# Performance work log

Hardware: AMD Instinct MI355X
Metric: run time of the kernel (lower is better)

Reference implementation:

```python
import jax, jax.numpy as jnp
import numpy as np

EPS = 1e-5
SLOPE = 0.01  # torch LeakyReLU default negative_slope


def _stage(h, W):
    # h: [B, N, k, Cin]; W: [Cout, Cin] (1x1 conv, no bias)
    h = jnp.einsum('bnkc,oc->bnko', h, W)
    # InstanceNorm2d (affine=False): normalize per (batch, channel) over spatial (N, k)
    mean = jnp.mean(h, axis=(1, 2), keepdims=True)
    var = jnp.var(h, axis=(1, 2), keepdims=True)
    h = (h - mean) * jax.lax.rsqrt(var + EPS)
    return jnp.where(h >= 0, h, SLOPE * h)


def setup_inputs() -> dict:
    key = jax.random.key(0)
    k1, k2, k3, k4, k5 = jax.random.split(key, 5)
    B, N, D, K, C = 8, 4096, 64, 20, 64
    x = jax.random.normal(k1, (B, N, D), dtype=jnp.float32)
    ind = jax.random.randint(k2, (B, N, K), 0, B * N, dtype=jnp.int64)
    W1 = jax.random.normal(k3, (C, 2 * D), dtype=jnp.float32) * 0.05
    W2 = jax.random.normal(k4, (C, C), dtype=jnp.float32) * 0.05
    W3 = jax.random.normal(k5, (C, C), dtype=jnp.float32) * 0.05
    return {"x": x, "ind": ind, "W1": W1, "W2": W2, "W3": W3}


def reference(x, ind, W1, W2, W3):
    B, N, D = x.shape
    k = ind.shape[2]
    # Gather neighbors via global (B*N) indices, as in the torch code
    y = x.reshape(B * N, D)[ind.reshape(B * N, k)].reshape(B, N, k, D)  # [B,N,k,D]
    xe = jnp.broadcast_to(x[:, :, None, :], (B, N, k, D))
    feat = jnp.concatenate([y - xe, xe], axis=3)  # [B,N,k,2D]
    h = _stage(feat, W1)
    h = _stage(h, W2)
    h = _stage(h, W3)
    # max-pool over k neighbors -> [B, N, Cout]
    return jnp.max(h, axis=2)
```

## Files before the change

kernel.cpp:

```cpp
#include <hip/hip_runtime.h>

#define BDIM 8
#define NPTS 4096
#define KNEI 20
#define BN (BDIM*NPTS)
#define NKCNT (NPTS*KNEI)
#define EPSI 1e-5f
#define SLOPE 0.01f

typedef _Float16 half_t;
typedef __attribute__((ext_vector_type(2))) _Float16 h2v;
typedef __attribute__((ext_vector_type(4))) _Float16 h4v;
typedef __attribute__((ext_vector_type(8))) _Float16 h8v;
typedef __attribute__((ext_vector_type(4))) float f32x4;
typedef __attribute__((ext_vector_type(2))) float f32x2;

__device__ __forceinline__ h2v cvt2(float a, float b) {
    return __builtin_bit_cast(h2v, __builtin_amdgcn_cvt_pkrtz(a, b));
}
__device__ __forceinline__ unsigned long long pack4_f16(const f32x4& a) {
    unsigned p0 = __builtin_bit_cast(unsigned, cvt2(a[0], a[1]));
    unsigned p1 = __builtin_bit_cast(unsigned, cvt2(a[2], a[3]));
    return ((unsigned long long)p1 << 32) | p0;
}

__global__ __launch_bounds__(256) void k0_uv(const float* __restrict__ x,
        const float* __restrict__ W1, const float* __restrict__ W2,
        const float* __restrict__ W3, half_t* __restrict__ u,
        half_t* __restrict__ v, half_t* __restrict__ Wh2,
        half_t* __restrict__ Wh3) {
    int tid = threadIdx.x;
    if (blockIdx.x >= BN / 16) {
        const float* src = (blockIdx.x == BN / 16) ? W2 : W3;
        half_t* dst = (blockIdx.x == BN / 16) ? Wh2 : Wh3;
        for (int i = tid; i < 4096; i += 256) dst[i] = (half_t)src[i];
        return;
    }
    __shared__ float wlds[64 * 129];
    __shared__ float xs[16 * 64];
    int m0 = blockIdx.x * 16;
    for (int i = tid; i < 8192; i += 256)
        wlds[(i >> 7) * 129 + (i & 127)] = W1[i];
    for (int i = tid; i < 1024; i += 256)
        xs[i] = x[m0 * 64 + i];
    __syncthreads();
    int o = tid & 63;
    int r0 = tid >> 6;
    float au[4] = {0.f, 0.f, 0.f, 0.f};
    float av[4] = {0.f, 0.f, 0.f, 0.f};
    for (int c = 0; c < 64; ++c) {
        float wa = wlds[o * 129 + c];
        float wb = wlds[o * 129 + 64 + c];
        float wd = wb - wa;
#pragma unroll
        for (int jj = 0; jj < 4; ++jj) {
            float xv = xs[(r0 + jj * 4) * 64 + c];
            au[jj] += xv * wa;
            av[jj] += xv * wd;
        }
    }
#pragma unroll
    for (int jj = 0; jj < 4; ++jj) {
        int m = m0 + r0 + jj * 4;
        u[(size_t)m * 64 + o] = (half_t)au[jj];
        v[(size_t)m * 64 + o] = (half_t)av[jj];
    }
}

__global__ __launch_bounds__(256) void k1_stats1(const half_t* __restrict__ u,
        const half_t* __restrict__ v, const int* __restrict__ ind,
        float* __restrict__ s1) {
    __shared__ float sacc[128];
    int tid = threadIdx.x;
    if (tid < 128) sacc[tid] = 0.f;
    int lane = tid & 63, w = tid >> 6;
    int b = blockIdx.x >> 8;
    int n0 = (blockIdx.x & 255) << 4;
    int p = b * NPTS + n0 + w * 4 + (lane >> 4);
    int rh = (lane >> 3) & 1, c8 = lane & 7;
    h8v vv = *(const h8v*)(v + (size_t)p * 64 + c8 * 8);
    const int* ip = ind + (size_t)p * 20;
    float s[8] = {}, qa[8] = {};
#pragma unroll
    for (int r = 0; r < 10; ++r) {
        int idx = ip[r * 2 + rh];
        h8v uu = *(const h8v*)(u + (size_t)idx * 64 + c8 * 8);
        h8v h = uu + vv;
#pragma unroll
        for (int j = 0; j < 8; ++j) {
            float f = (float)h[j];
            s[j] += f; qa[j] = fmaf(f, f, qa[j]);
        }
    }
#pragma unroll
    for (int m = 8; m <= 32; m <<= 1)
#pragma unroll
        for (int j = 0; j < 8; ++j) {
            s[j] += __shfl_xor(s[j], m, 64);
            qa[j] += __shfl_xor(qa[j], m, 64);
        }
    __syncthreads();
    if ((lane & 56) == 0) {
#pragma unroll
        for (int j = 0; j < 8; ++j) {
            atomicAdd(&sacc[c8 * 8 + j], s[j]);
            atomicAdd(&sacc[64 + c8 * 8 + j], qa[j]);
        }
    }
    __syncthreads();
    if (tid < 128)
        atomicAdd(&s1[(tid >> 6) * 512 + b * 64 + (tid & 63)], sacc[tid]);
}

__global__ __launch_bounds__(256, 4) void k2_stats2(const half_t* __restrict__ u,
        const half_t* __restrict__ v, const int* __restrict__ ind,
        const half_t* __restrict__ Wh2, const float* __restrict__ s1,
        float* __restrict__ s2) {
    __shared__ float sacc[128];
    int tid = threadIdx.x;
    if (tid < 128) sacc[tid] = 0.f;
    int lane = tid & 63, w = tid >> 6;
    int l15 = lane & 15, q = lane >> 4;
    int b = blockIdx.x >> 8;
    int n0 = (blockIdx.x & 255) << 4;
    int base = b * NPTS + n0;
    int base20 = base * 20;
    h8v aw[4][2];
#pragma unroll
    for (int mt = 0; mt < 4; ++mt)
#pragma unroll
        for (int kc = 0; kc < 2; ++kc)
            aw[mt][kc] = *(const h8v*)(Wh2 + (mt * 16 + l15) * 64 + kc * 32 + q * 8);
    const float inv = 1.0f / (float)NKCNT;
    h8v r1v[2], m1v[2];
#pragma unroll
    for (int kc = 0; kc < 2; ++kc)
#pragma unroll
        for (int j = 0; j < 8; ++j) {
            int c = kc * 32 + q * 8 + j;
            float mm = s1[b * 64 + c] * inv;
            float va = s1[512 + b * 64 + c] * inv - mm * mm;
            float rs = rsqrtf(va + EPSI);
            r1v[kc][j] = (half_t)rs;
            m1v[kc][j] = (half_t)(-mm * rs);
        }
    int gp = base + w * 4 + (l15 >> 2);
    h8v vfr[2];
#pragma unroll
    for (int kc = 0; kc < 2; ++kc)
        vfr[kc] = *(const h8v*)(v + (size_t)gp * 64 + kc * 32 + q * 8);
    int idxs[5];
#pragma unroll
    for (int nt = 0; nt < 5; ++nt)
        idxs[nt] = ind[base20 + w * 80 + l15 * 5 + nt];
    float ss[4][4] = {}, sq[4][4] = {};
#pragma unroll
    for (int nt = 0; nt < 5; ++nt) {
        const half_t* up = u + (size_t)idxs[nt] * 64;
        h8v bfr[2];
#pragma unroll
        for (int kc = 0; kc < 2; ++kc) {
            h8v uu = *(const h8v*)(up + kc * 32 + q * 8);
            h8v h = uu + vfr[kc];
            h8v t = h * r1v[kc] + m1v[kc];
            bfr[kc] = __builtin_elementwise_max(t, t * (half_t)SLOPE);
        }
#pragma unroll
        for (int mt = 0; mt < 4; ++mt) {
            f32x4 a = {0.f, 0.f, 0.f, 0.f};
            a = __builtin_amdgcn_mfma_f32_16x16x32_f16(aw[mt][0], bfr[0], a, 0, 0, 0);
            a = __builtin_amdgcn_mfma_f32_16x16x32_f16(aw[mt][1], bfr[1], a, 0, 0, 0);
#pragma unroll
            for (int j = 0; j < 4; ++j) {
                ss[mt][j] += a[j];
                sq[mt][j] = fmaf(a[j], a[j], sq[mt][j]);
            }
        }
    }
#pragma unroll
    for (int m = 1; m < 16; m <<= 1)
#pragma unroll
        for (int mt = 0; mt < 4; ++mt)
#pragma unroll
            for (int j = 0; j < 4; ++j) {
                ss[mt][j] += __shfl_xor(ss[mt][j], m, 64);
                sq[mt][j] += __shfl_xor(sq[mt][j], m, 64);
            }
    __syncthreads();
    if (l15 == 0) {
#pragma unroll
        for (int mt = 0; mt < 4; ++mt)
#pragma unroll
            for (int j = 0; j < 4; ++j) {
                atomicAdd(&sacc[mt * 16 + q * 4 + j], ss[mt][j]);
                atomicAdd(&sacc[64 + mt * 16 + q * 4 + j], sq[mt][j]);
            }
    }
    __syncthreads();
    if (tid < 128)
        atomicAdd(&s2[(tid >> 6) * 512 + b * 64 + (tid & 63)], sacc[tid]);
}

__global__ __launch_bounds__(256, 4) void k3_fused(const half_t* __restrict__ u,
        const half_t* __restrict__ v, const int* __restrict__ ind,
        const half_t* __restrict__ Wh2, const half_t* __restrict__ Wh3,
        const float* __restrict__ s1, const float* __restrict__ s2,
        float* __restrict__ s3, float* __restrict__ out) {
    __shared__ __align__(16) unsigned char wlds[16384];
    __shared__ __align__(16) unsigned char scr[16384];
    __shared__ float sacc[128];
    int tid = threadIdx.x;
    if (tid < 128) sacc[tid] = 0.f;
    int lane = tid & 63, w = tid >> 6;
    int l15 = lane & 15, q = lane >> 4;
    int rw7 = l15 & 7;
    int b = blockIdx.x >> 8;
    int n0 = (blockIdx.x & 255) << 4;
    int base = b * NPTS + n0;
    int base20 = base * 20;
    for (int i = tid; i < 512; i += 256) {
        int rw = i >> 3, ch = i & 7;
        *(h8v*)(wlds + rw * 128 + ((ch ^ (rw & 7)) << 4)) =
            *(const h8v*)(Wh2 + rw * 64 + ch * 8);
        *(h8v*)(wlds + 8192 + rw * 128 + ((ch ^ (rw & 7)) << 4)) =
            *(const h8v*)(Wh3 + rw * 64 + ch * 8);
    }
    const float inv = 1.0f / (float)NKCNT;
    h8v r1v[2], m1v[2], r2v[2], m2v[2];
#pragma unroll
    for (int kc = 0; kc < 2; ++kc)
#pragma unroll
        for (int j = 0; j < 8; ++j) {
            int c = kc * 32 + q * 8 + j;
            float mm = s1[b * 64 + c] * inv;
            float va = s1[512 + b * 64 + c] * inv - mm * mm;
            float rs = rsqrtf(va + EPSI);
            r1v[kc][j] = (half_t)rs;
            m1v[kc][j] = (half_t)(-mm * rs);
            float mm2 = s2[b * 64 + c] * inv;
            float va2 = s2[512 + b * 64 + c] * inv - mm2 * mm2;
            float rs2 = rsqrtf(va2 + EPSI);
            r2v[kc][j] = (half_t)rs2;
            m2v[kc][j] = (half_t)(-mm2 * rs2);
        }
    int gp = base + w * 4 + (l15 >> 2);
    h8v vfr[2];
#pragma unroll
    for (int kc = 0; kc < 2; ++kc)
        vfr[kc] = *(const h8v*)(v + (size_t)gp * 64 + kc * 32 + q * 8);
    int idxs[5];
#pragma unroll
    for (int nt = 0; nt < 5; ++nt)
        idxs[nt] = ind[base20 + w * 80 + l15 * 5 + nt];
    __syncthreads();
    h8v bf2[5][2];
#pragma unroll
    for (int nt = 0; nt < 5; ++nt) {
        unsigned char* scrw = scr + w * 4096 + (nt & 1) * 2048;
        const half_t* up = u + (size_t)idxs[nt] * 64;
        h8v bfr[2];
#pragma unroll
        for (int kc = 0; kc < 2; ++kc) {
            h8v uu = *(const h8v*)(up + kc * 32 + q * 8);
            h8v h = uu + vfr[kc];
            h8v t = h * r1v[kc] + m1v[kc];
            bfr[kc] = __builtin_elementwise_max(t, t * (half_t)SLOPE);
        }
#pragma unroll
        for (int mt = 0; mt < 4; ++mt) {
            h8v w0 = *(const h8v*)(wlds + (mt * 16 + l15) * 128 + ((q ^ rw7) << 4));
            h8v w1 = *(const h8v*)(wlds + (mt * 16 + l15) * 128 + (((4 + q) ^ rw7) << 4));
            f32x4 a = {0.f, 0.f, 0.f, 0.f};
            a = __builtin_amdgcn_mfma_f32_16x16x32_f16(w0, bfr[0], a, 0, 0, 0);
            a = __builtin_amdgcn_mfma_f32_16x16x32_f16(w1, bfr[1], a, 0, 0, 0);
            *(unsigned long long*)(scrw + l15 * 128 +
                (((mt * 2 + (q >> 1)) ^ rw7) << 4) + (q & 1) * 8) = pack4_f16(a);
        }
#pragma unroll
        for (int kc = 0; kc < 2; ++kc) {
            h8v hv = *(const h8v*)(scrw + l15 * 128 + (((kc * 4 + q) ^ rw7) << 4));
            h8v t = hv * r2v[kc] + m2v[kc];
            bf2[nt][kc] = __builtin_elementwise_max(t, t * (half_t)SLOPE);
        }
    }
    float ss[4][4] = {}, sq[4][4] = {};
    h2v pm[4][2];
#pragma unroll
    for (int mt = 0; mt < 4; ++mt)
#pragma unroll
        for (int r = 0; r < 2; ++r)
            pm[mt][r] = (h2v){(half_t)-65504.f, (half_t)-65504.f};
#pragma unroll
    for (int nt = 0; nt < 5; ++nt) {
#pragma unroll
        for (int mt = 0; mt < 4; ++mt) {
            h8v w0 = *(const h8v*)(wlds + 8192 + (mt * 16 + l15) * 128 + ((q ^ rw7) << 4));
            h8v w1 = *(const h8v*)(wlds + 8192 + (mt * 16 + l15) * 128 + (((4 + q) ^ rw7) << 4));
            f32x4 a = {0.f, 0.f, 0.f, 0.f};
            a = __builtin_amdgcn_mfma_f32_16x16x32_f16(w0, bf2[nt][0], a, 0, 0, 0);
            a = __builtin_amdgcn_mfma_f32_16x16x32_f16(w1, bf2[nt][1], a, 0, 0, 0);
#pragma unroll
            for (int j = 0; j < 4; ++j) {
                ss[mt][j] += a[j];
                sq[mt][j] = fmaf(a[j], a[j], sq[mt][j]);
            }
            h2v p0 = cvt2(a[0], a[1]);
            h2v p1 = cvt2(a[2], a[3]);
            pm[mt][0] = __builtin_elementwise_max(pm[mt][0], p0);
            pm[mt][1] = __builtin_elementwise_max(pm[mt][1], p1);
        }
    }
#pragma unroll
    for (int m = 1; m <= 2; m <<= 1)
#pragma unroll
        for (int mt = 0; mt < 4; ++mt)
#pragma unroll
            for (int r = 0; r < 2; ++r) {
                int t = __shfl_xor(__builtin_bit_cast(int, pm[mt][r]), m, 64);
                pm[mt][r] = __builtin_elementwise_max(pm[mt][r],
                               __builtin_bit_cast(h2v, t));
            }
    {
        int ms = l15 & 3;
        h2v sa = ms == 0 ? pm[0][0] : ms == 1 ? pm[1][0] : ms == 2 ? pm[2][0] : pm[3][0];
        h2v sb = ms == 0 ? pm[0][1] : ms == 1 ? pm[1][1] : ms == 2 ? pm[2][1] : pm[3][1];
        f32x4 o = {(float)sa[0], (float)sa[1], (float)sb[0], (float)sb[1]};
        *(f32x4*)(out + (size_t)gp * 64 + ms * 16 + q * 4) = o;
    }
#pragma unroll
    for (int m = 1; m < 16; m <<= 1)
#pragma unroll
        for (int mt = 0; mt < 4; ++mt)
#pragma unroll
            for (int j = 0; j < 4; ++j) {
                ss[mt][j] += __shfl_xor(ss[mt][j], m, 64);
                sq[mt][j] += __shfl_xor(sq[mt][j], m, 64);
            }
    if (l15 == 0) {
#pragma unroll
        for (int mt = 0; mt < 4; ++mt)
#pragma unroll
            for (int j = 0; j < 4; ++j) {
                atomicAdd(&sacc[mt * 16 + q * 4 + j], ss[mt][j]);
                atomicAdd(&sacc[64 + mt * 16 + q * 4 + j], sq[mt][j]);
            }
    }
    __syncthreads();
    if (tid < 128)
        atomicAdd(&s3[(tid >> 6) * 512 + b * 64 + (tid & 63)], sacc[tid]);
}

__global__ __launch_bounds__(256) void k4_final(float* __restrict__ out,
        const float* __restrict__ s3) {
    int idx = blockIdx.x * 256 + threadIdx.x;
    int c = idx & 63;
    int b = idx >> 18;
    const float inv = 1.0f / (float)NKCNT;
    float mm = s3[b * 64 + c] * inv;
    float vv = s3[512 + b * 64 + c] * inv - mm * mm;
    float r = rsqrtf(vv + EPSI);
    float val = (out[idx] - mm) * r;
    out[idx] = val >= 0.f ? val : SLOPE * val;
}

extern "C" void kernel_launch(void* const* d_in, const int* in_sizes, int n_in,
                              void* d_out, int out_size, void* d_ws, size_t ws_size,
                              hipStream_t stream) {
    const float* x   = (const float*)d_in[0];
    const int*   ind = (const int*)d_in[1];
    const float* W1  = (const float*)d_in[2];
    const float* W2  = (const float*)d_in[3];
    const float* W3  = (const float*)d_in[4];
    float* out = (float*)d_out;

    half_t* u   = (half_t*)d_ws;
    half_t* v   = u + (size_t)BN * 64;
    half_t* Wh2 = v + (size_t)BN * 64;
    half_t* Wh3 = Wh2 + 4096;
    float* stats = (float*)(Wh3 + 4096);
    float* s1 = stats;
    float* s2 = stats + 1024;
    float* s3 = stats + 2048;

    (void)hipMemsetAsync(stats, 0, 3 * 1024 * sizeof(float), stream);
    k0_uv<<<dim3(BN / 16 + 2), dim3(256), 0, stream>>>(x, W1, W2, W3, u, v, Wh2, Wh3);
    k1_stats1<<<dim3(BN / 16), dim3(256), 0, stream>>>(u, v, ind, s1);
    k2_stats2<<<dim3(BN / 16), dim3(256), 0, stream>>>(u, v, ind, Wh2, s1, s2);
    k3_fused<<<dim3(BN / 16), dim3(256), 0, stream>>>(u, v, ind, Wh2, Wh3, s1, s2, s3, out);
    k4_final<<<dim3(BN * 64 / 256), dim3(256), 0, stream>>>(out, s3);
}
```

Measured before the change: 185.6 us.

## Use MFMA for u/v precompute, batch gathers, keep weights in registers

After: 192.3 us. 1.04x slower.

```diff
diff --git a/kernel.cpp b/kernel.cpp
--- a/kernel.cpp
+++ b/kernel.cpp
@@ -30,40 +30,53 @@
         half_t* __restrict__ v, half_t* __restrict__ Wh2,
         half_t* __restrict__ Wh3) {
     int tid = threadIdx.x;
-    if (blockIdx.x >= BN / 16) {
-        const float* src = (blockIdx.x == BN / 16) ? W2 : W3;
-        half_t* dst = (blockIdx.x == BN / 16) ? Wh2 : Wh3;
+    if (blockIdx.x >= BN / 64) {
+        const float* src = (blockIdx.x == BN / 64) ? W2 : W3;
+        half_t* dst = (blockIdx.x == BN / 64) ? Wh2 : Wh3;
         for (int i = tid; i < 4096; i += 256) dst[i] = (half_t)src[i];
         return;
     }
-    __shared__ float wlds[64 * 129];
-    __shared__ float xs[16 * 64];
-    int m0 = blockIdx.x * 16;
-    for (int i = tid; i < 8192; i += 256)
-        wlds[(i >> 7) * 129 + (i & 127)] = W1[i];
-    for (int i = tid; i < 1024; i += 256)
-        xs[i] = x[m0 * 64 + i];
-    __syncthreads();
-    int o = tid & 63;
-    int r0 = tid >> 6;
-    float au[4] = {0.f, 0.f, 0.f, 0.f};
-    float av[4] = {0.f, 0.f, 0.f, 0.f};
-    for (int c = 0; c < 64; ++c) {
-        float wa = wlds[o * 129 + c];
-        float wb = wlds[o * 129 + 64 + c];
-        float wd = wb - wa;
-#pragma unroll
-        for (int jj = 0; jj < 4; ++jj) {
-            float xv = xs[(r0 + jj * 4) * 64 + c];
-            au[jj] += xv * wa;
-            av[jj] += xv * wd;
-        }
-    }
-#pragma unroll
-    for (int jj = 0; jj < 4; ++jj) {
-        int m = m0 + r0 + jj * 4;
-        u[(size_t)m * 64 + o] = (half_t)au[jj];
-        v[(size_t)m * 64 + o] = (half_t)av[jj];
+    int lane = tid & 63, w = tid >> 6;
+    int l15 = lane & 15, q = lane >> 4;
+    int row = blockIdx.x * 64 + w * 16 + l15;
+    h8v bx[2];
+#pragma unroll
+    for (int kc = 0; kc < 2; ++kc) {
+        const float* xp = x + (size_t)row * 64 + kc * 32 + q * 8;
+        f32x4 x0 = *(const f32x4*)xp;
+        f32x4 x1 = *(const f32x4*)(xp + 4);
+        h8v t;
+#pragma unroll
+        for (int j = 0; j < 4; ++j) { t[j] = (half_t)x0[j]; t[4 + j] = (half_t)x1[j]; }
+        bx[kc] = t;
+    }
+    h8v wa[4][2], wd[4][2];
+#pragma unroll
+    for (int mt = 0; mt < 4; ++mt)
+#pragma unroll
+        for (int kc = 0; kc < 2; ++kc) {
+            const float* wp = W1 + (mt * 16 + l15) * 128 + kc * 32 + q * 8;
+            f32x4 a0 = *(const f32x4*)wp;
+            f32x4 a1 = *(const f32x4*)(wp + 4);
+            f32x4 b0 = *(const f32x4*)(wp + 64);
+            f32x4 b1 = *(const f32x4*)(wp + 68);
+            h8v ta, td;
+#pragma unroll
+            for (int j = 0; j < 4; ++j) {
+                ta[j] = (half_t)a0[j]; ta[4 + j] = (half_t)a1[j];
+                td[j] = (half_t)(b0[j] - a0[j]); td[4 + j] = (half_t)(b1[j] - a1[j]);
+            }
+            wa[mt][kc] = ta; wd[mt][kc] = td;
+        }
+#pragma unroll
+    for (int mt = 0; mt < 4; ++mt) {
+        f32x4 au = {0.f, 0.f, 0.f, 0.f}, av = {0.f, 0.f, 0.f, 0.f};
+        au = __builtin_amdgcn_mfma_f32_16x16x32_f16(wa[mt][0], bx[0], au, 0, 0, 0);
+        au = __builtin_amdgcn_mfma_f32_16x16x32_f16(wa[mt][1], bx[1], au, 0, 0, 0);
+        av = __builtin_amdgcn_mfma_f32_16x16x32_f16(wd[mt][0], bx[0], av, 0, 0, 0);
+        av = __builtin_amdgcn_mfma_f32_16x16x32_f16(wd[mt][1], bx[1], av, 0, 0, 0);
+        *(unsigned long long*)(u + (size_t)row * 64 + mt * 16 + q * 4) = pack4_f16(au);
+        *(unsigned long long*)(v + (size_t)row * 64 + mt * 16 + q * 4) = pack4_f16(av);
     }
 }
 
@@ -78,14 +91,19 @@
     int n0 = (blockIdx.x & 255) << 4;
     int p = b * NPTS + n0 + w * 4 + (lane >> 4);
     int rh = (lane >> 3) & 1, c8 = lane & 7;
+    const int* ip = ind + (size_t)p * 20;
+    int idx[10];
+#pragma unroll
+    for (int r = 0; r < 10; ++r) idx[r] = ip[r * 2 + rh];
     h8v vv = *(const h8v*)(v + (size_t)p * 64 + c8 * 8);
-    const int* ip = ind + (size_t)p * 20;
+    h8v g[10];
+#pragma unroll
+    for (int r = 0; r < 10; ++r)
+        g[r] = *(const h8v*)(u + (size_t)idx[r] * 64 + c8 * 8);
     float s[8] = {}, qa[8] = {};
 #pragma unroll
     for (int r = 0; r < 10; ++r) {
-        int idx = ip[r * 2 + rh];
-        h8v uu = *(const h8v*)(u + (size_t)idx * 64 + c8 * 8);
-        h8v h = uu + vv;
+        h8v h = g[r] + vv;
 #pragma unroll
         for (int j = 0; j < 8; ++j) {
             float f = (float)h[j];
@@ -125,6 +143,22 @@
     int n0 = (blockIdx.x & 255) << 4;
     int base = b * NPTS + n0;
     int base20 = base * 20;
+    int idxs[5];
+#pragma unroll
+    for (int nt = 0; nt < 5; ++nt)
+        idxs[nt] = ind[base20 + w * 80 + l15 * 5 + nt];
+    h8v ug[5][2];
+#pragma unroll
+    for (int nt = 0; nt < 5; ++nt) {
+        const half_t* up = u + (size_t)idxs[nt] * 64 + q * 8;
+        ug[nt][0] = *(const h8v*)up;
+        ug[nt][1] = *(const h8v*)(up + 32);
+    }
+    int gp = base + w * 4 + (l15 >> 2);
+    h8v vfr[2];
+#pragma unroll
+    for (int kc = 0; kc < 2; ++kc)
+        vfr[kc] = *(const h8v*)(v + (size_t)gp * 64 + kc * 32 + q * 8);
     h8v aw[4][2];
 #pragma unroll
     for (int mt = 0; mt < 4; ++mt)
@@ -132,7 +166,7 @@
         for (int kc = 0; kc < 2; ++kc)
             aw[mt][kc] = *(const h8v*)(Wh2 + (mt * 16 + l15) * 64 + kc * 32 + q * 8);
     const float inv = 1.0f / (float)NKCNT;
-    h8v r1v[2], m1v[2];
+    h8v r1v[2], vn[2];
 #pragma unroll
     for (int kc = 0; kc < 2; ++kc)
 #pragma unroll
@@ -142,27 +176,15 @@
             float va = s1[512 + b * 64 + c] * inv - mm * mm;
             float rs = rsqrtf(va + EPSI);
             r1v[kc][j] = (half_t)rs;
-            m1v[kc][j] = (half_t)(-mm * rs);
-        }
-    int gp = base + w * 4 + (l15 >> 2);
-    h8v vfr[2];
-#pragma unroll
-    for (int kc = 0; kc < 2; ++kc)
-        vfr[kc] = *(const h8v*)(v + (size_t)gp * 64 + kc * 32 + q * 8);
-    int idxs[5];
-#pragma unroll
-    for (int nt = 0; nt < 5; ++nt)
-        idxs[nt] = ind[base20 + w * 80 + l15 * 5 + nt];
+            vn[kc][j] = (half_t)(((float)vfr[kc][j] - mm) * rs);
+        }
     float ss[4][4] = {}, sq[4][4] = {};
 #pragma unroll
     for (int nt = 0; nt < 5; ++nt) {
-        const half_t* up = u + (size_t)idxs[nt] * 64;
         h8v bfr[2];
 #pragma unroll
         for (int kc = 0; kc < 2; ++kc) {
-            h8v uu = *(const h8v*)(up + kc * 32 + q * 8);
-            h8v h = uu + vfr[kc];
-            h8v t = h * r1v[kc] + m1v[kc];
+            h8v t = ug[nt][kc] * r1v[kc] + vn[kc];
             bfr[kc] = __builtin_elementwise_max(t, t * (half_t)SLOPE);
         }
 #pragma unroll
@@ -206,7 +228,6 @@
         const half_t* __restrict__ Wh2, const half_t* __restrict__ Wh3,
         const float* __restrict__ s1, const float* __restrict__ s2,
         float* __restrict__ s3, float* __restrict__ out) {
-    __shared__ __align__(16) unsigned char wlds[16384];
     __shared__ __align__(16) unsigned char scr[16384];
     __shared__ float sacc[128];
     int tid = threadIdx.x;
@@ -218,15 +239,26 @@
     int n0 = (blockIdx.x & 255) << 4;
     int base = b * NPTS + n0;
     int base20 = base * 20;
-    for (int i = tid; i < 512; i += 256) {
-        int rw = i >> 3, ch = i & 7;
-        *(h8v*)(wlds + rw * 128 + ((ch ^ (rw & 7)) << 4)) =
-            *(const h8v*)(Wh2 + rw * 64 + ch * 8);
-        *(h8v*)(wlds + 8192 + rw * 128 + ((ch ^ (rw & 7)) << 4)) =
-            *(const h8v*)(Wh3 + rw * 64 + ch * 8);
-    }
+    int idxs[5];
+#pragma unroll
+    for (int nt = 0; nt < 5; ++nt)
+        idxs[nt] = ind[base20 + w * 80 + l15 * 5 + nt];
+    const half_t* up0 = u + (size_t)idxs[0] * 64 + q * 8;
+    h8v ua = *(const h8v*)up0;
+    h8v ub = *(const h8v*)(up0 + 32);
+    int gp = base + w * 4 + (l15 >> 2);
+    h8v vfr[2];
+#pragma unroll
+    for (int kc = 0; kc < 2; ++kc)
+        vfr[kc] = *(const h8v*)(v + (size_t)gp * 64 + kc * 32 + q * 8);
+    h8v aw2[4][2];
+#pragma unroll
+    for (int mt = 0; mt < 4; ++mt)
+#pragma unroll
+        for (int kc = 0; kc < 2; ++kc)
+            aw2[mt][kc] = *(const h8v*)(Wh2 + (mt * 16 + l15) * 64 + kc * 32 + q * 8);
     const float inv = 1.0f / (float)NKCNT;
-    h8v r1v[2], m1v[2], r2v[2], m2v[2];
+    h8v r1v[2], vn[2];
 #pragma unroll
     for (int kc = 0; kc < 2; ++kc)
 #pragma unroll
@@ -236,53 +268,56 @@
             float va = s1[512 + b * 64 + c] * inv - mm * mm;
             float rs = rsqrtf(va + EPSI);
             r1v[kc][j] = (half_t)rs;
-            m1v[kc][j] = (half_t)(-mm * rs);
+            vn[kc][j] = (half_t)(((float)vfr[kc][j] - mm) * rs);
+        }
+    unsigned char* scrw0 = scr + w * 4096;
+    h8v bf2[5][2];
+#pragma unroll
+    for (int nt = 0; nt < 5; ++nt) {
+        h8v cu0 = ua, cu1 = ub;
+        if (nt < 4) {
+            const half_t* upn = u + (size_t)idxs[nt + 1] * 64 + q * 8;
+            ua = *(const h8v*)upn;
+            ub = *(const h8v*)(upn + 32);
+        }
+        unsigned char* scrw = scrw0 + (nt & 1) * 2048;
+        h8v bfr[2];
+        {
+            h8v t0 = cu0 * r1v[0] + vn[0];
+            h8v t1 = cu1 * r1v[1] + vn[1];
+            bfr[0] = __builtin_elementwise_max(t0, t0 * (half_t)SLOPE);
+            bfr[1] = __builtin_elementwise_max(t1, t1 * (half_t)SLOPE);
+        }
+#pragma unroll
+        for (int mt = 0; mt < 4; ++mt) {
+            f32x4 a = {0.f, 0.f, 0.f, 0.f};
+            a = __builtin_amdgcn_mfma_f32_16x16x32_f16(aw2[mt][0], bfr[0], a, 0, 0, 0);
+            a = __builtin_amdgcn_mfma_f32_16x16x32_f16(aw2[mt][1], bfr[1], a, 0, 0, 0);
+            *(unsigned long long*)(scrw + l15 * 128 +
+                (((mt * 2 + (q >> 1)) ^ rw7) << 4) + (q & 1) * 8) = pack4_f16(a);
+        }
+#pragma unroll
+        for (int kc = 0; kc < 2; ++kc)
+            bf2[nt][kc] = *(const h8v*)(scrw + l15 * 128 + (((kc * 4 + q) ^ rw7) << 4));
+    }
+    h8v aw3[4][2];
+#pragma unroll
+    for (int mt = 0; mt < 4; ++mt)
+#pragma unroll
+        for (int kc = 0; kc < 2; ++kc)
+            aw3[mt][kc] = *(const h8v*)(Wh3 + (mt * 16 + l15) * 64 + kc * 32 + q * 8);
+    h8v r2v[2], m2v[2];
+#pragma unroll
+    for (int kc = 0; kc < 2; ++kc)
+#pragma unroll
+        for (int j = 0; j < 8; ++j) {
+            int c = kc * 32 + q * 8 + j;
             float mm2 = s2[b * 64 + c] * inv;
             float va2 = s2[512 + b * 64 + c] * inv - mm2 * mm2;
             float rs2 = rsqrtf(va2 + EPSI);
             r2v[kc][j] = (half_t)rs2;
             m2v[kc][j] = (half_t)(-mm2 * rs2);
         }
-    int gp = base + w * 4 + (l15 >> 2);
-    h8v vfr[2];
-#pragma unroll
-    for (int kc = 0; kc < 2; ++kc)
-        vfr[kc] = *(const h8v*)(v + (size_t)gp * 64 + kc * 32 + q * 8);
-    int idxs[5];
-#pragma unroll
-    for (int nt = 0; nt < 5; ++nt)
-        idxs[nt] = ind[base20 + w * 80 + l15 * 5 + nt];
-    __syncthreads();
-    h8v bf2[5][2];
-#pragma unroll
-    for (int nt = 0; nt < 5; ++nt) {
-        unsigned char* scrw = scr + w * 4096 + (nt & 1) * 2048;
-        const half_t* up = u + (size_t)idxs[nt] * 64;
-        h8v bfr[2];
-#pragma unroll
-        for (int kc = 0; kc < 2; ++kc) {
-            h8v uu = *(const h8v*)(up + kc * 32 + q * 8);
-            h8v h = uu + vfr[kc];
-            h8v t = h * r1v[kc] + m1v[kc];
-            bfr[kc] = __builtin_elementwise_max(t, t * (half_t)SLOPE);
-        }
-#pragma unroll
-        for (int mt = 0; mt < 4; ++mt) {
-            h8v w0 = *(const h8v*)(wlds + (mt * 16 + l15) * 128 + ((q ^ rw7) << 4));
-            h8v w1 = *(const h8v*)(wlds + (mt * 16 + l15) * 128 + (((4 + q) ^ rw7) << 4));
-            f32x4 a = {0.f, 0.f, 0.f, 0.f};
-            a = __builtin_amdgcn_mfma_f32_16x16x32_f16(w0, bfr[0], a, 0, 0, 0);
-            a = __builtin_amdgcn_mfma_f32_16x16x32_f16(w1, bfr[1], a, 0, 0, 0);
-            *(unsigned long long*)(scrw + l15 * 128 +
-                (((mt * 2 + (q >> 1)) ^ rw7) << 4) + (q & 1) * 8) = pack4_f16(a);
-        }
-#pragma unroll
-        for (int kc = 0; kc < 2; ++kc) {
-            h8v hv = *(const h8v*)(scrw + l15 * 128 + (((kc * 4 + q) ^ rw7) << 4));
-            h8v t = hv * r2v[kc] + m2v[kc];
-            bf2[nt][kc] = __builtin_elementwise_max(t, t * (half_t)SLOPE);
-        }
-    }
     float ss[4][4] = {}, sq[4][4] = {};
     h2v pm[4][2];
 #pragma unroll
@@ -292,13 +327,18 @@
             pm[mt][r] = (h2v){(half_t)-65504.f, (half_t)-65504.f};
 #pragma unroll
     for (int nt = 0; nt < 5; ++nt) {
+        h8v b0, b1;
+        {
+            h8v t0 = bf2[nt][0] * r2v[0] + m2v[0];
+            h8v t1 = bf2[nt][1] * r2v[1] + m2v[1];
+            b0 = __builtin_elementwise_max(t0, t0 * (half_t)SLOPE);
+            b1 = __builtin_elementwise_max(t1, t1 * (half_t)SLOPE);
+        }
 #pragma unroll
         for (int mt = 0; mt < 4; ++mt) {
-            h8v w0 = *(const h8v*)(wlds + 8192 + (mt * 16 + l15) * 128 + ((q ^ rw7) << 4));
-            h8v w1 = *(const h8v*)(wlds + 8192 + (mt * 16 + l15) * 128 + (((4 + q) ^ rw7) << 4));
             f32x4 a = {0.f, 0.f, 0.f, 0.f};
-            a = __builtin_amdgcn_mfma_f32_16x16x32_f16(w0, bf2[nt][0], a, 0, 0, 0);
-            a = __builtin_amdgcn_mfma_f32_16x16x32_f16(w1, bf2[nt][1], a, 0, 0, 0);
+            a = __builtin_amdgcn_mfma_f32_16x16x32_f16(aw3[mt][0], b0, a, 0, 0, 0);
+            a = __builtin_amdgcn_mfma_f32_16x16x32_f16(aw3[mt][1], b1, a, 0, 0, 0);
 #pragma unroll
             for (int j = 0; j < 4; ++j) {
                 ss[mt][j] += a[j];
@@ -336,6 +376,7 @@
                 ss[mt][j] += __shfl_xor(ss[mt][j], m, 64);
                 sq[mt][j] += __shfl_xor(sq[mt][j], m, 64);
             }
+    __syncthreads();
     if (l15 == 0) {
 #pragma unroll
         for (int mt = 0; mt < 4; ++mt)
@@ -383,7 +424,7 @@
     float* s3 = stats + 2048;
 
     (void)hipMemsetAsync(stats, 0, 3 * 1024 * sizeof(float), stream);
-    k0_uv<<<dim3(BN / 16 + 2), dim3(256), 0, stream>>>(x, W1, W2, W3, u, v, Wh2, Wh3);
+    k0_uv<<<dim3(BN / 64 + 2), dim3(256), 0, stream>>>(x, W1, W2, W3, u, v, Wh2, Wh3);
     k1_stats1<<<dim3(BN / 16), dim3(256), 0, stream>>>(u, v, ind, s1);
     k2_stats2<<<dim3(BN / 16), dim3(256), 0, stream>>>(u, v, ind, Wh2, s1, s2);
     k3_fused<<<dim3(BN / 16), dim3(256), 0, stream>>>(u, v, ind, Wh2, Wh3, s1, s2, s3, out);
```
